# Optimization experiments

Hardware: AMD Instinct MI355X
Metric: run time of the kernel (lower is better)

The kernel has to match this reference:

```python
import jax, jax.numpy as jnp
import numpy as np

N = 1024      # num_nodes
D = 64        # node_embedding_dim
H = 64        # hidden_dim
LN_EPS = 1e-5


def setup_inputs() -> dict:
    key = jax.random.key(0)
    ks = jax.random.split(key, 6)
    node_embeddings = jax.random.normal(ks[0], (N, D), dtype=jnp.float32)
    valid_mask = jax.random.randint(ks[1], (N * N,), 0, 2).astype(jnp.float32)
    s1 = 1.0 / np.sqrt(2 * D)
    s2 = 1.0 / np.sqrt(H)
    W1 = jax.random.normal(ks[2], (2 * D, H), dtype=jnp.float32) * s1
    b1 = jnp.zeros((H,), jnp.float32)
    g1 = jnp.ones((H,), jnp.float32)
    be1 = jnp.zeros((H,), jnp.float32)
    W2 = jax.random.normal(ks[3], (H, H), dtype=jnp.float32) * s2
    b2 = jnp.zeros((H,), jnp.float32)
    g2 = jnp.ones((H,), jnp.float32)
    be2 = jnp.zeros((H,), jnp.float32)
    W3 = jax.random.normal(ks[4], (H, 1), dtype=jnp.float32) * s2
    b3 = jnp.zeros((1,), jnp.float32)
    return {
        "node_embeddings": node_embeddings, "valid_mask": valid_mask,
        "W1": W1, "b1": b1, "g1": g1, "be1": be1,
        "W2": W2, "b2": b2, "g2": g2, "be2": be2,
        "W3": W3, "b3": b3,
    }


def _layer_norm(x, g, b):
    m = jnp.mean(x, axis=-1, keepdims=True)
    v = jnp.mean((x - m) ** 2, axis=-1, keepdims=True)
    return (x - m) * jax.lax.rsqrt(v + LN_EPS) * g + b


def reference(node_embeddings, valid_mask, W1, b1, g1, be1, W2, b2, g2, be2, W3, b3):
    n, d = node_embeddings.shape
    # Build all ordered pairs (i, j): concat([emb_i, emb_j]) -> [n*n, 2d]
    src = jnp.broadcast_to(node_embeddings[:, None, :], (n, n, d))
    tgt = jnp.broadcast_to(node_embeddings[None, :, :], (n, n, d))
    e = jnp.concatenate([src, tgt], axis=-1).reshape(n * n, 2 * d)
    # MLP: Linear -> LayerNorm -> ReLU (x2 hidden) -> Linear(1)
    h = jax.nn.relu(_layer_norm(e @ W1 + b1, g1, be1))
    h = jax.nn.relu(_layer_norm(h @ W2 + b2, g2, be2))
    scores = (h @ W3 + b3)[:, 0]  # [n*n]
    # Original never scores self-edges (i == j) and multiplies by valid_mask.
    off_diag = 1.0 - jnp.eye(n, dtype=scores.dtype).reshape(-1)
    return scores * valid_mask * off_diag
```

## Files before the change

### kernel.cpp

```cpp
#include <hip/hip_runtime.h>
#include <hip/hip_bf16.h>

#define NN 1024
#define LN_EPS 1e-5f

typedef __bf16 bf16x8 __attribute__((ext_vector_type(8)));
typedef float floatx16 __attribute__((ext_vector_type(16)));
typedef float floatx4 __attribute__((ext_vector_type(4)));
typedef float floatx2 __attribute__((ext_vector_type(2)));

__global__ __launch_bounds__(256) void precompute_ab(
    const float* __restrict__ emb, const float* __restrict__ W1,
    const float* __restrict__ b1, const float* __restrict__ W2,
    float* __restrict__ Ap, float* __restrict__ Bp,
    float* __restrict__ sumA, float* __restrict__ sumB,
    __bf16* __restrict__ Wf) {
    if (blockIdx.x == 1024) {
        int tid = threadIdx.x;
        if (tid >= 64) return;
        int m_l = tid & 31, kg = tid >> 5;
#pragma unroll
        for (int mt = 0; mt < 2; mt++)
#pragma unroll
            for (int s = 0; s < 4; s++) {
                bf16x8 f;
#pragma unroll
                for (int t = 0; t < 8; t++) {
                    int k = s * 16 + kg * 8 + t;
                    f[t] = (__bf16)W2[k * 64 + mt * 32 + m_l];
                }
                *(bf16x8*)&Wf[((mt * 4 + s) * 64 + tid) * 8] = f;
            }
        return;
    }
    __shared__ __align__(16) float e[64];
    __shared__ float pA[4][64], pB[4][64];
    int i = blockIdx.x;
    int h = threadIdx.x & 63, q = threadIdx.x >> 6;
    if (threadIdx.x < 64) e[h] = emb[i * 64 + h];
    __syncthreads();
    float a = 0.f, b = 0.f;
#pragma unroll
    for (int dd = 0; dd < 16; dd++) {
        int d = q * 16 + dd;
        a = fmaf(e[d], W1[d * 64 + h], a);
        b = fmaf(e[d], W1[(64 + d) * 64 + h], b);
    }
    pA[q][h] = a;
    pB[q][h] = b;
    __syncthreads();
    if (threadIdx.x < 64) {
        float ra = pA[0][h] + pA[1][h] + pA[2][h] + pA[3][h] + b1[h];
        float rb = pB[0][h] + pB[1][h] + pB[2][h] + pB[3][h];
        Ap[i * 64 + h] = ra;
        Bp[i * 64 + h] = rb;
#pragma unroll
        for (int off = 1; off < 64; off <<= 1) {
            ra += __shfl_xor(ra, off);
            rb += __shfl_xor(rb, off);
        }
        if (h == 0) { sumA[i] = ra; sumB[i] = rb; }
    }
}

__global__ __launch_bounds__(256, 4) void fused(
    const float* __restrict__ Ap, const float* __restrict__ Bp, const __bf16* __restrict__ Wf,
    const float* __restrict__ sumA, const float* __restrict__ sumB,
    const float* __restrict__ g1, const float* __restrict__ be1, const float* __restrict__ b2,
    const float* __restrict__ g2, const float* __restrict__ be2, const float* __restrict__ W3,
    const float* __restrict__ b3, const float* __restrict__ mask, float* __restrict__ out) {
    __shared__ __align__(16) float B2s[64], G2s[64], BE2s[64], W3s[64];
    __shared__ __align__(16) __bf16 h1t[4][64 * 64];

    int tid = threadIdx.x;
    int wave = tid >> 6, lane = tid & 63;
    int i = blockIdx.x >> 2;
    int j0 = (blockIdx.x & 3) * 256 + wave * 64;

    if (tid < 64) {
        B2s[tid] = b2[tid]; G2s[tid] = g2[tid];
        BE2s[tid] = be2[tid]; W3s[tid] = W3[tid];
    }
    __syncthreads();

    int j = j0 + lane;
    float sBj = sumB[j];
    const floatx4* bp4 = (const floatx4*)(Bp + j * 64);
    const floatx4* ap4 = (const floatx4*)(Ap + i * 64);
    floatx2 x2[32];
    floatx2 qa = {0.f, 0.f}, qb = {0.f, 0.f};
#pragma unroll
    for (int c = 0; c < 16; c++) {
        floatx4 bb = bp4[c];
        floatx4 aa = ap4[c];
        floatx2 v0 = {aa[0] + bb[0], aa[1] + bb[1]};
        floatx2 v1 = {aa[2] + bb[2], aa[3] + bb[3]};
        x2[2 * c] = v0;
        x2[2 * c + 1] = v1;
        qa += v0 * v0;
        qb += v1 * v1;
    }
    floatx2 qs = qa + qb;
    float sq = qs[0] + qs[1];
    float m1 = (sumA[i] + sBj) * 0.015625f;
    float var1 = fmaf(m1, -m1, sq * 0.015625f);
    float rs1 = rsqrtf(var1 + LN_EPS);
    floatx2 p1 = {rs1, rs1};
    float ofs = -m1 * rs1;
    floatx2 o1 = {ofs, ofs};

    __bf16* rowp = &h1t[wave][lane * 64];
    int sw = lane & 7;
#pragma unroll
    for (int c = 0; c < 8; c++) {
        bf16x8 fr;
#pragma unroll
        for (int t = 0; t < 4; t++) {
            floatx2 gg = *(const floatx2*)&g1[c * 8 + 2 * t];
            floatx2 ee = *(const floatx2*)&be1[c * 8 + 2 * t];
            floatx2 xn = x2[c * 4 + t] * p1 + o1;
            floatx2 y = xn * gg + ee;
            y = __builtin_elementwise_max(y, (floatx2){0.f, 0.f});
            fr[2 * t] = (__bf16)y[0];
            fr[2 * t + 1] = (__bf16)y[1];
        }
        *(bf16x8*)(rowp + ((c ^ sw) * 8)) = fr;
    }
    asm volatile("s_waitcnt lgkmcnt(0)" ::: "memory");

    int m_l = lane & 31, kg2 = lane >> 5;
    bf16x8 afrag[2][4];
#pragma unroll
    for (int mt = 0; mt < 2; mt++)
#pragma unroll
        for (int s = 0; s < 4; s++)
            afrag[mt][s] = *(const bf16x8*)&Wf[((mt * 4 + s) * 64 + lane) * 8];

    floatx16 acc[2][2];
#pragma unroll
    for (int a = 0; a < 2; a++)
#pragma unroll
        for (int b = 0; b < 2; b++)
#pragma unroll
            for (int r = 0; r < 16; r++) acc[a][b][r] = 0.f;

    const __bf16* wbase = &h1t[wave][0];
#pragma unroll
    for (int nt = 0; nt < 2; nt++) {
        int pair = nt * 32 + m_l;
#pragma unroll
        for (int s = 0; s < 4; s++) {
            int chunk = s * 2 + kg2;
            bf16x8 bfrag = *(const bf16x8*)(wbase + pair * 64 + ((chunk ^ (pair & 7)) * 8));
#pragma unroll
            for (int mt = 0; mt < 2; mt++)
                acc[mt][nt] = __builtin_amdgcn_mfma_f32_32x32x16_bf16(
                    afrag[mt][s], bfrag, acc[mt][nt], 0, 0, 0);
        }
    }

    float b3v = b3[0];

#pragma unroll
    for (int nt = 0; nt < 2; nt++) {
        floatx2 s2v = {0.f, 0.f}, q2v = {0.f, 0.f};
#pragma unroll
        for (int mt = 0; mt < 2; mt++) {
#pragma unroll
            for (int q = 0; q < 4; q++) {
                int r0 = mt * 32 + q * 8 + kg2 * 4;
                floatx4 bq = *(const floatx4*)&B2s[r0];
                floatx2 vlo = {acc[mt][nt][q * 4 + 0] + bq[0], acc[mt][nt][q * 4 + 1] + bq[1]};
                floatx2 vhi = {acc[mt][nt][q * 4 + 2] + bq[2], acc[mt][nt][q * 4 + 3] + bq[3]};
                acc[mt][nt][q * 4 + 0] = vlo[0]; acc[mt][nt][q * 4 + 1] = vlo[1];
                acc[mt][nt][q * 4 + 2] = vhi[0]; acc[mt][nt][q * 4 + 3] = vhi[1];
                s2v += vlo; s2v += vhi;
                q2v += vlo * vlo; q2v += vhi * vhi;
            }
        }
        float s2 = s2v[0] + s2v[1];
        float q2 = q2v[0] + q2v[1];
        s2 += __shfl_xor(s2, 32);
        q2 += __shfl_xor(q2, 32);
        float m2 = s2 * 0.015625f;
        float var2 = fmaf(m2, -m2, q2 * 0.015625f);
        float rs2 = rsqrtf(var2 + LN_EPS);
        floatx2 p2 = {rs2, rs2};
        float o2s = -m2 * rs2;
        floatx2 o2 = {o2s, o2s};

        floatx2 scv = {0.f, 0.f};
#pragma unroll
        for (int mt = 0; mt < 2; mt++) {
#pragma unroll
            for (int q = 0; q < 4; q++) {
                int r0 = mt * 32 + q * 8 + kg2 * 4;
                floatx4 gq = *(const floatx4*)&G2s[r0];
                floatx4 eq = *(const floatx4*)&BE2s[r0];
                floatx4 wq = *(const floatx4*)&W3s[r0];
                floatx2 vlo = {acc[mt][nt][q * 4 + 0], acc[mt][nt][q * 4 + 1]};
                floatx2 vhi = {acc[mt][nt][q * 4 + 2], acc[mt][nt][q * 4 + 3]};
                floatx2 xlo = vlo * p2 + o2;
                floatx2 xhi = vhi * p2 + o2;
                floatx2 ylo = xlo * (floatx2){gq[0], gq[1]} + (floatx2){eq[0], eq[1]};
                floatx2 yhi = xhi * (floatx2){gq[2], gq[3]} + (floatx2){eq[2], eq[3]};
                ylo = __builtin_elementwise_max(ylo, (floatx2){0.f, 0.f});
                yhi = __builtin_elementwise_max(yhi, (floatx2){0.f, 0.f});
                scv += ylo * (floatx2){wq[0], wq[1]};
                scv += yhi * (floatx2){wq[2], wq[3]};
            }
        }
        float sc = scv[0] + scv[1];
        sc += __shfl_xor(sc, 32);

        if (kg2 == 0) {
            int jj = j0 + nt * 32 + m_l;
            int p = i * NN + jj;
            out[p] = (i == jj) ? 0.f : (sc + b3v) * mask[p];
        }
    }
}

extern "C" void kernel_launch(void* const* d_in, const int* in_sizes, int n_in,
                              void* d_out, int out_size, void* d_ws, size_t ws_size,
                              hipStream_t stream) {
    const float* emb = (const float*)d_in[0];
    const float* mask = (const float*)d_in[1];
    const float* W1 = (const float*)d_in[2];
    const float* b1 = (const float*)d_in[3];
    const float* g1 = (const float*)d_in[4];
    const float* be1 = (const float*)d_in[5];
    const float* W2 = (const float*)d_in[6];
    const float* b2 = (const float*)d_in[7];
    const float* g2 = (const float*)d_in[8];
    const float* be2 = (const float*)d_in[9];
    const float* W3 = (const float*)d_in[10];
    const float* b3 = (const float*)d_in[11];
    float* out = (float*)d_out;

    float* Ap = (float*)d_ws;
    float* Bp = Ap + 1024 * 64;
    float* sA = Bp + 1024 * 64;
    float* sB = sA + 1024;
    __bf16* Wf = (__bf16*)(sB + 1024);

    precompute_ab<<<1025, 256, 0, stream>>>(emb, W1, b1, W2, Ap, Bp, sA, sB, Wf);
    fused<<<4096, 256, 0, stream>>>(Ap, Bp, Wf, sA, sB, g1, be1, b2, g2, be2, W3, b3, mask, out);
}
```

Measured before the change: 123.3 us.

## Build layer-2 MFMA operands in registers and compute LN1 variance via dot-product MFMA

The fused kernel now stages a 128-row tile of Bp into LDS with global_load_lds, then builds the bf16 B operand of the W2 MFMA directly in registers. This drops the round trip that wrote layer-1 activations to LDS and read them back. The LayerNorm-1 variance is expanded as |a|^2 + 2a·b + |b|^2. The precompute kernel now supplies the squared norms, and the cross term a·b comes from a bf16 MFMA. Each wave handles 32 pairs instead of 64 and the grid doubles to 8192 blocks. The bf16 cross term can lose precision in the variance through cancellation.

```diff
diff --git a/kernel.cpp b/kernel.cpp
--- a/kernel.cpp
+++ b/kernel.cpp
@@ -8,12 +8,19 @@
 typedef float floatx16 __attribute__((ext_vector_type(16)));
 typedef float floatx4 __attribute__((ext_vector_type(4)));
 typedef float floatx2 __attribute__((ext_vector_type(2)));
+
+__device__ __forceinline__ void load_lds16(const float* g, float* l) {
+    __builtin_amdgcn_global_load_lds(
+        (const __attribute__((address_space(1))) void*)g,
+        (__attribute__((address_space(3))) void*)l, 16, 0, 0);
+}
 
 __global__ __launch_bounds__(256) void precompute_ab(
     const float* __restrict__ emb, const float* __restrict__ W1,
     const float* __restrict__ b1, const float* __restrict__ W2,
     float* __restrict__ Ap, float* __restrict__ Bp,
     float* __restrict__ sumA, float* __restrict__ sumB,
+    float* __restrict__ sqA, float* __restrict__ sqB,
     __bf16* __restrict__ Wf) {
     if (blockIdx.x == 1024) {
         int tid = threadIdx.x;
@@ -54,170 +61,187 @@
         float rb = pB[0][h] + pB[1][h] + pB[2][h] + pB[3][h];
         Ap[i * 64 + h] = ra;
         Bp[i * 64 + h] = rb;
+        float qa = ra * ra, qb = rb * rb;
 #pragma unroll
         for (int off = 1; off < 64; off <<= 1) {
             ra += __shfl_xor(ra, off);
             rb += __shfl_xor(rb, off);
-        }
-        if (h == 0) { sumA[i] = ra; sumB[i] = rb; }
+            qa += __shfl_xor(qa, off);
+            qb += __shfl_xor(qb, off);
+        }
+        if (h == 0) { sumA[i] = ra; sumB[i] = rb; sqA[i] = qa; sqB[i] = qb; }
     }
 }
 
 __global__ __launch_bounds__(256, 4) void fused(
     const float* __restrict__ Ap, const float* __restrict__ Bp, const __bf16* __restrict__ Wf,
     const float* __restrict__ sumA, const float* __restrict__ sumB,
+    const float* __restrict__ sqA, const float* __restrict__ sqB,
     const float* __restrict__ g1, const float* __restrict__ be1, const float* __restrict__ b2,
     const float* __restrict__ g2, const float* __restrict__ be2, const float* __restrict__ W3,
     const float* __restrict__ b3, const float* __restrict__ mask, float* __restrict__ out) {
-    __shared__ __align__(16) float B2s[64], G2s[64], BE2s[64], W3s[64];
-    __shared__ __align__(16) __bf16 h1t[4][64 * 64];
+    __shared__ __align__(16) float Bt[128 * 64];
+    __shared__ __align__(16) float A_s[64], G1s[64], E1s[64], B2s[64], G2s[64], E2s[64], W3s[64];
 
     int tid = threadIdx.x;
     int wave = tid >> 6, lane = tid & 63;
-    int i = blockIdx.x >> 2;
-    int j0 = (blockIdx.x & 3) * 256 + wave * 64;
-
+    int i = blockIdx.x >> 3;
+    int j0 = (blockIdx.x & 7) * 128;
+
+    {
+        int cp = lane & 15;
+#pragma unroll
+        for (int o = 0; o < 8; o++) {
+            int rr = wave * 32 + o * 4 + (lane >> 4);
+            int cs = (cp & 8) | ((cp & 7) ^ (rr & 7));
+            load_lds16(Bp + (j0 + rr) * 64 + cs * 4, Bt + (wave * 8 + o) * 256);
+        }
+    }
     if (tid < 64) {
-        B2s[tid] = b2[tid]; G2s[tid] = g2[tid];
-        BE2s[tid] = be2[tid]; W3s[tid] = W3[tid];
+        A_s[tid] = Ap[i * 64 + tid];
+        G1s[tid] = g1[tid]; E1s[tid] = be1[tid];
+        B2s[tid] = b2[tid]; G2s[tid] = g2[tid]; E2s[tid] = be2[tid];
+        W3s[tid] = W3[tid];
     }
     __syncthreads();
 
-    int j = j0 + lane;
-    float sBj = sumB[j];
-    const floatx4* bp4 = (const floatx4*)(Bp + j * 64);
-    const floatx4* ap4 = (const floatx4*)(Ap + i * 64);
-    floatx2 x2[32];
-    floatx2 qa = {0.f, 0.f}, qb = {0.f, 0.f};
-#pragma unroll
-    for (int c = 0; c < 16; c++) {
-        floatx4 bb = bp4[c];
-        floatx4 aa = ap4[c];
-        floatx2 v0 = {aa[0] + bb[0], aa[1] + bb[1]};
-        floatx2 v1 = {aa[2] + bb[2], aa[3] + bb[3]};
-        x2[2 * c] = v0;
-        x2[2 * c + 1] = v1;
-        qa += v0 * v0;
-        qb += v1 * v1;
-    }
-    floatx2 qs = qa + qb;
-    float sq = qs[0] + qs[1];
-    float m1 = (sumA[i] + sBj) * 0.015625f;
-    float var1 = fmaf(m1, -m1, sq * 0.015625f);
+    int m_l = lane & 31, kg2 = lane >> 5;
+    int myp = wave * 32 + m_l;
+    int myj = j0 + myp;
+
+    float sBj = sumB[myj], qBj = sqB[myj];
+    float sAi = sumA[i], qAi = sqA[i];
+    float b3v = b3[0];
+
+    floatx4 gr[4][2];
+    const float* trow = Bt + myp * 64;
+#pragma unroll
+    for (int s = 0; s < 4; s++) {
+        int c0 = s * 4 + kg2 * 2;
+#pragma unroll
+        for (int q = 0; q < 2; q++) {
+            int c = c0 + q;
+            int sp = (c & 8) | ((c & 7) ^ (myp & 7));
+            gr[s][q] = *(const floatx4*)(trow + sp * 4);
+        }
+    }
+
+    bf16x8 afragD[4];
+#pragma unroll
+    for (int s = 0; s < 4; s++) {
+        floatx4 a0 = *(const floatx4*)(A_s + s * 16 + kg2 * 8);
+        floatx4 a1 = *(const floatx4*)(A_s + s * 16 + kg2 * 8 + 4);
+#pragma unroll
+        for (int t = 0; t < 4; t++) { afragD[s][t] = (__bf16)a0[t]; afragD[s][4 + t] = (__bf16)a1[t]; }
+    }
+    floatx16 accD;
+#pragma unroll
+    for (int r = 0; r < 16; r++) accD[r] = 0.f;
+#pragma unroll
+    for (int s = 0; s < 4; s++) {
+        bf16x8 bd;
+#pragma unroll
+        for (int q = 0; q < 2; q++)
+#pragma unroll
+            for (int t = 0; t < 4; t++) bd[q * 4 + t] = (__bf16)gr[s][q][t];
+        accD = __builtin_amdgcn_mfma_f32_32x32x16_bf16(afragD[s], bd, accD, 0, 0, 0);
+    }
+
+    bf16x8 afragW[2][4];
+#pragma unroll
+    for (int mt = 0; mt < 2; mt++)
+#pragma unroll
+        for (int s = 0; s < 4; s++)
+            afragW[mt][s] = *(const bf16x8*)&Wf[((mt * 4 + s) * 64 + lane) * 8];
+
+    float dot = accD[0];
+    float m1 = (sAi + sBj) * 0.015625f;
+    float var1 = fmaf(m1, -m1, (qAi + 2.f * dot + qBj) * 0.015625f);
     float rs1 = rsqrtf(var1 + LN_EPS);
-    floatx2 p1 = {rs1, rs1};
-    float ofs = -m1 * rs1;
-    floatx2 o1 = {ofs, ofs};
-
-    __bf16* rowp = &h1t[wave][lane * 64];
-    int sw = lane & 7;
-#pragma unroll
-    for (int c = 0; c < 8; c++) {
-        bf16x8 fr;
-#pragma unroll
-        for (int t = 0; t < 4; t++) {
-            floatx2 gg = *(const floatx2*)&g1[c * 8 + 2 * t];
-            floatx2 ee = *(const floatx2*)&be1[c * 8 + 2 * t];
-            floatx2 xn = x2[c * 4 + t] * p1 + o1;
-            floatx2 y = xn * gg + ee;
-            y = __builtin_elementwise_max(y, (floatx2){0.f, 0.f});
-            fr[2 * t] = (__bf16)y[0];
-            fr[2 * t + 1] = (__bf16)y[1];
-        }
-        *(bf16x8*)(rowp + ((c ^ sw) * 8)) = fr;
-    }
-    asm volatile("s_waitcnt lgkmcnt(0)" ::: "memory");
-
-    int m_l = lane & 31, kg2 = lane >> 5;
-    bf16x8 afrag[2][4];
-#pragma unroll
-    for (int mt = 0; mt < 2; mt++)
-#pragma unroll
-        for (int s = 0; s < 4; s++)
-            afrag[mt][s] = *(const bf16x8*)&Wf[((mt * 4 + s) * 64 + lane) * 8];
-
-    floatx16 acc[2][2];
-#pragma unroll
-    for (int a = 0; a < 2; a++)
-#pragma unroll
-        for (int b = 0; b < 2; b++)
-#pragma unroll
-            for (int r = 0; r < 16; r++) acc[a][b][r] = 0.f;
-
-    const __bf16* wbase = &h1t[wave][0];
-#pragma unroll
-    for (int nt = 0; nt < 2; nt++) {
-        int pair = nt * 32 + m_l;
-#pragma unroll
-        for (int s = 0; s < 4; s++) {
-            int chunk = s * 2 + kg2;
-            bf16x8 bfrag = *(const bf16x8*)(wbase + pair * 64 + ((chunk ^ (pair & 7)) * 8));
-#pragma unroll
-            for (int mt = 0; mt < 2; mt++)
-                acc[mt][nt] = __builtin_amdgcn_mfma_f32_32x32x16_bf16(
-                    afrag[mt][s], bfrag, acc[mt][nt], 0, 0, 0);
-        }
-    }
-
-    float b3v = b3[0];
-
-#pragma unroll
-    for (int nt = 0; nt < 2; nt++) {
-        floatx2 s2v = {0.f, 0.f}, q2v = {0.f, 0.f};
-#pragma unroll
-        for (int mt = 0; mt < 2; mt++) {
-#pragma unroll
-            for (int q = 0; q < 4; q++) {
-                int r0 = mt * 32 + q * 8 + kg2 * 4;
-                floatx4 bq = *(const floatx4*)&B2s[r0];
-                floatx2 vlo = {acc[mt][nt][q * 4 + 0] + bq[0], acc[mt][nt][q * 4 + 1] + bq[1]};
-                floatx2 vhi = {acc[mt][nt][q * 4 + 2] + bq[2], acc[mt][nt][q * 4 + 3] + bq[3]};
-                acc[mt][nt][q * 4 + 0] = vlo[0]; acc[mt][nt][q * 4 + 1] = vlo[1];
-                acc[mt][nt][q * 4 + 2] = vhi[0]; acc[mt][nt][q * 4 + 3] = vhi[1];
-                s2v += vlo; s2v += vhi;
-                q2v += vlo * vlo; q2v += vhi * vhi;
+    float o1 = -m1 * rs1;
+    floatx2 p1v = {rs1, rs1}, o1v = {o1, o1};
+
+    floatx16 acc0, acc1;
+#pragma unroll
+    for (int r = 0; r < 16; r++) { acc0[r] = 0.f; acc1[r] = 0.f; }
+
+#pragma unroll
+    for (int s = 0; s < 4; s++) {
+        bf16x8 bh;
+#pragma unroll
+        for (int q = 0; q < 2; q++) {
+            floatx4 aq = *(const floatx4*)(A_s + s * 16 + kg2 * 8 + q * 4);
+            floatx4 gq = *(const floatx4*)(G1s + s * 16 + kg2 * 8 + q * 4);
+            floatx4 eq = *(const floatx4*)(E1s + s * 16 + kg2 * 8 + q * 4);
+#pragma unroll
+            for (int t2 = 0; t2 < 2; t2++) {
+                floatx2 x = {gr[s][q][2 * t2] + aq[2 * t2], gr[s][q][2 * t2 + 1] + aq[2 * t2 + 1]};
+                floatx2 xn = x * p1v + o1v;
+                floatx2 y = xn * (floatx2){gq[2 * t2], gq[2 * t2 + 1]} +
+                            (floatx2){eq[2 * t2], eq[2 * t2 + 1]};
+                y = __builtin_elementwise_max(y, (floatx2){0.f, 0.f});
+                bh[q * 4 + 2 * t2] = (__bf16)y[0];
+                bh[q * 4 + 2 * t2 + 1] = (__bf16)y[1];
             }
         }
-        float s2 = s2v[0] + s2v[1];
-        float q2 = q2v[0] + q2v[1];
-        s2 += __shfl_xor(s2, 32);
-        q2 += __shfl_xor(q2, 32);
-        float m2 = s2 * 0.015625f;
-        float var2 = fmaf(m2, -m2, q2 * 0.015625f);
-        float rs2 = rsqrtf(var2 + LN_EPS);
-        floatx2 p2 = {rs2, rs2};
-        float o2s = -m2 * rs2;
-        floatx2 o2 = {o2s, o2s};
-
-        floatx2 scv = {0.f, 0.f};
-#pragma unroll
-        for (int mt = 0; mt < 2; mt++) {
-#pragma unroll
-            for (int q = 0; q < 4; q++) {
-                int r0 = mt * 32 + q * 8 + kg2 * 4;
-                floatx4 gq = *(const floatx4*)&G2s[r0];
-                floatx4 eq = *(const floatx4*)&BE2s[r0];
-                floatx4 wq = *(const floatx4*)&W3s[r0];
-                floatx2 vlo = {acc[mt][nt][q * 4 + 0], acc[mt][nt][q * 4 + 1]};
-                floatx2 vhi = {acc[mt][nt][q * 4 + 2], acc[mt][nt][q * 4 + 3]};
-                floatx2 xlo = vlo * p2 + o2;
-                floatx2 xhi = vhi * p2 + o2;
-                floatx2 ylo = xlo * (floatx2){gq[0], gq[1]} + (floatx2){eq[0], eq[1]};
-                floatx2 yhi = xhi * (floatx2){gq[2], gq[3]} + (floatx2){eq[2], eq[3]};
-                ylo = __builtin_elementwise_max(ylo, (floatx2){0.f, 0.f});
-                yhi = __builtin_elementwise_max(yhi, (floatx2){0.f, 0.f});
-                scv += ylo * (floatx2){wq[0], wq[1]};
-                scv += yhi * (floatx2){wq[2], wq[3]};
-            }
-        }
-        float sc = scv[0] + scv[1];
-        sc += __shfl_xor(sc, 32);
-
-        if (kg2 == 0) {
-            int jj = j0 + nt * 32 + m_l;
-            int p = i * NN + jj;
-            out[p] = (i == jj) ? 0.f : (sc + b3v) * mask[p];
-        }
+        acc0 = __builtin_amdgcn_mfma_f32_32x32x16_bf16(afragW[0][s], bh, acc0, 0, 0, 0);
+        acc1 = __builtin_amdgcn_mfma_f32_32x32x16_bf16(afragW[1][s], bh, acc1, 0, 0, 0);
+    }
+
+    floatx2 s2v = {0.f, 0.f}, q2v = {0.f, 0.f};
+#pragma unroll
+    for (int mt = 0; mt < 2; mt++) {
+        floatx16& A = mt ? acc1 : acc0;
+#pragma unroll
+        for (int q = 0; q < 4; q++) {
+            int r0 = mt * 32 + q * 8 + kg2 * 4;
+            floatx4 bq = *(const floatx4*)&B2s[r0];
+            floatx2 vlo = {A[q * 4 + 0] + bq[0], A[q * 4 + 1] + bq[1]};
+            floatx2 vhi = {A[q * 4 + 2] + bq[2], A[q * 4 + 3] + bq[3]};
+            A[q * 4 + 0] = vlo[0]; A[q * 4 + 1] = vlo[1];
+            A[q * 4 + 2] = vhi[0]; A[q * 4 + 3] = vhi[1];
+            s2v += vlo; s2v += vhi;
+            q2v += vlo * vlo; q2v += vhi * vhi;
+        }
+    }
+    float s2 = s2v[0] + s2v[1], q2 = q2v[0] + q2v[1];
+    s2 += __shfl_xor(s2, 32);
+    q2 += __shfl_xor(q2, 32);
+    float m2 = s2 * 0.015625f;
+    float var2 = fmaf(m2, -m2, q2 * 0.015625f);
+    float rs2 = rsqrtf(var2 + LN_EPS);
+    floatx2 p2 = {rs2, rs2};
+    float o2s = -m2 * rs2;
+    floatx2 o2 = {o2s, o2s};
+
+    floatx2 scv = {0.f, 0.f};
+#pragma unroll
+    for (int mt = 0; mt < 2; mt++) {
+        floatx16& A = mt ? acc1 : acc0;
+#pragma unroll
+        for (int q = 0; q < 4; q++) {
+            int r0 = mt * 32 + q * 8 + kg2 * 4;
+            floatx4 gq = *(const floatx4*)&G2s[r0];
+            floatx4 eq = *(const floatx4*)&E2s[r0];
+            floatx4 wq = *(const floatx4*)&W3s[r0];
+            floatx2 vlo = {A[q * 4 + 0], A[q * 4 + 1]};
+            floatx2 vhi = {A[q * 4 + 2], A[q * 4 + 3]};
+            floatx2 xlo = vlo * p2 + o2;
+            floatx2 xhi = vhi * p2 + o2;
+            floatx2 ylo = xlo * (floatx2){gq[0], gq[1]} + (floatx2){eq[0], eq[1]};
+            floatx2 yhi = xhi * (floatx2){gq[2], gq[3]} + (floatx2){eq[2], eq[3]};
+            ylo = __builtin_elementwise_max(ylo, (floatx2){0.f, 0.f});
+            yhi = __builtin_elementwise_max(yhi, (floatx2){0.f, 0.f});
+            scv += ylo * (floatx2){wq[0], wq[1]};
+            scv += yhi * (floatx2){wq[2], wq[3]};
+        }
+    }
+    float sc = scv[0] + scv[1];
+    sc += __shfl_xor(sc, 32);
+
+    if (kg2 == 0) {
+        int p = i * NN + myj;
+        out[p] = (i == myj) ? 0.f : (sc + b3v) * mask[p];
     }
 }
 
@@ -242,8 +266,11 @@
     float* Bp = Ap + 1024 * 64;
     float* sA = Bp + 1024 * 64;
     float* sB = sA + 1024;
-    __bf16* Wf = (__bf16*)(sB + 1024);
-
-    precompute_ab<<<1025, 256, 0, stream>>>(emb, W1, b1, W2, Ap, Bp, sA, sB, Wf);
-    fused<<<4096, 256, 0, stream>>>(Ap, Bp, Wf, sA, sB, g1, be1, b2, g2, be2, W3, b3, mask, out);
-}
+    float* qA = sB + 1024;
+    float* qB = qA + 1024;
+    __bf16* Wf = (__bf16*)(qB + 1024);
+
+    precompute_ab<<<1025, 256, 0, stream>>>(emb, W1, b1, W2, Ap, Bp, sA, sB, qA, qB, Wf);
+    fused<<<8192, 256, 0, stream>>>(Ap, Bp, Wf, sA, sB, qA, qB,
+                                    g1, be1, b2, g2, be2, W3, b3, mask, out);
+}
```

Result: faster. 113.8 us (-7.7%).
